# Kernel optimization log

Measured on AMD Instinct MI355X. Metric: run time of the kernel, lower is better.

The kernel has to match this reference:

```python
import jax, jax.numpy as jnp
import numpy as np

WS = 3          # windows_size
ND = 3          # num_dilation, dilations [1,2,3]
NSTATE = 16     # d_state
RANK = 12       # dt_rank = ceil(192/16)
TOPK = 36       # max(1,(20//3)**2)*depth
DM = 192        # d_model
DI = 384        # d_inner = 2*d_model
B0, HH, WW = 8, 96, 96


def setup_inputs() -> dict:
    ks = jax.random.split(jax.random.key(0), 12)
    f = jax.random.normal
    return {
        "x": f(ks[0], (B0, HH, WW, DM), jnp.float32),
        "W_in": f(ks[1], (2 * DI, DM), jnp.float32) * 0.02,
        "conv_w": f(ks[2], (DI, 1, 7, 7), jnp.float32) * 0.05,
        "conv_b": f(ks[3], (DI,), jnp.float32) * 0.01,
        "x_proj_w": f(ks[4], (2, RANK + 2 * NSTATE, DI), jnp.float32) * 0.02,
        "dt_w": f(ks[5], (2, DI, RANK), jnp.float32) * 0.02,
        "dt_b": f(ks[6], (2, DI), jnp.float32) * 0.01,
        "A_logs": jnp.tile(jnp.log(jnp.arange(1, NSTATE + 1, dtype=jnp.float32)), (2 * DI, 1)),
        "Ds": jnp.ones((2 * DI,), jnp.float32),
        "W_kv": f(ks[7], (2 * DI, DI), jnp.float32) * 0.02,
        "b_kv": jnp.zeros((2 * DI,), jnp.float32),
        "ln_g": jnp.ones((DI,), jnp.float32),
        "ln_b": jnp.zeros((DI,), jnp.float32),
        "W_out": f(ks[8], (DM, DI), jnp.float32) * 0.02,
    }


def _selective_scan(xs, x_proj_w, dt_w, dt_b, A_logs, Ds):
    # xs: (B, K=2, D, L) -> (B, K, D, L). Standard Mamba selective scan.
    B, K, D, L = xs.shape
    x_dbl = jnp.einsum('bkdl,kcd->bkcl', xs, x_proj_w)          # (B,K,R+2N,L)
    dts = x_dbl[:, :, :RANK]
    Bs = x_dbl[:, :, RANK:RANK + NSTATE]                        # (B,K,N,L)
    Cs = x_dbl[:, :, RANK + NSTATE:]                            # (B,K,N,L)
    delta = jax.nn.softplus(jnp.einsum('bkrl,kdr->bkdl', dts, dt_w) + dt_b[None, :, :, None])
    A = -jnp.exp(A_logs).reshape(K, D, NSTATE)
    dA = jnp.exp(delta[..., None] * A[None, :, :, None, :])    # (B,K,D,L,N)
    dBu = delta[..., None] * Bs.transpose(0, 1, 3, 2)[:, :, None, :, :] * xs[..., None]
    dA = jnp.moveaxis(dA, 3, 0)                                 # (L,B,K,D,N)
    dBu = jnp.moveaxis(dBu, 3, 0)
    C = jnp.moveaxis(Cs, 3, 0)                                  # (L,B,K,N)

    def step(h, inp):
        dA_t, dBu_t, C_t = inp
        h = dA_t * h + dBu_t
        y = jnp.einsum('bkdn,bkn->bkd', h, C_t)
        return h, y

    h0 = jnp.zeros((B, K, D, NSTATE), xs.dtype)
    _, ys = jax.lax.scan(step, h0, (dA, dBu, C))                # ys: (L,B,K,D)
    y = jnp.moveaxis(ys, 0, 3)                                  # (B,K,D,L)
    return y + Ds.reshape(1, K, D, 1) * xs


def _dynamic_mask_active(x):
    # x: (B,D,H,W). Partition into WSxWS windows, keep TOPK by mean activation.
    B, D, H, W = x.shape
    nH, nW = H // WS, W // WS
    w = x.reshape(B, D, nH, WS, nW, WS).transpose(0, 2, 4, 1, 3, 5)
    w = w.reshape(B, nH * nW, D, WS * WS)                       # (B,nWin,D,ws2)
    score = w.mean(axis=(2, 3))                                 # (B,nWin)
    _, idx = jax.lax.top_k(score, TOPK)                         # (B,TOPK)
    g = jnp.take_along_axis(w, idx[:, :, None, None], axis=1)   # (B,TOPK,D,ws2)
    return g.transpose(0, 2, 1, 3).reshape(B, D, TOPK * WS * WS)


def _unfold(x, d):
    # torch nn.Unfold(kernel=WS, dilation=d, padding=d, stride=1) on (B,C,H,W)
    B, C, H, W = x.shape
    xp = jnp.pad(x, ((0, 0), (0, 0), (d, d), (d, d)))
    pats = [xp[:, :, i * d:i * d + H, j * d:j * d + W] for i in range(WS) for j in range(WS)]
    p = jnp.stack(pats, axis=2)                                 # (B,C,ws2,H,W) channel-major like torch
    return p.reshape(B, C, WS * WS, H * W)


def _forward(x, W_in, conv_w, conv_b, x_proj_w, dt_w, dt_b, A_logs, Ds,
             W_kv, b_kv, ln_g, ln_b, W_out):
    B, H, W_, _ = x.shape
    xz = jnp.einsum('bhwc,oc->bhwo', x, W_in)
    xf, z = jnp.split(xz, 2, axis=-1)                           # (B,H,W,DI) each
    xc = xf.transpose(0, 3, 1, 2)
    xc = jax.lax.conv_general_dilated(xc, conv_w, (1, 1), [(3, 3), (3, 3)],
                                      feature_group_count=conv_w.shape[0],
                                      dimension_numbers=('NCHW', 'OIHW', 'NCHW'))
    xc = xc + conv_b[None, :, None, None]                       # (B,DI,H,W)
    D = xc.shape[1]

    # foreground SSM on active windows (forward + flipped scan)
    act = _dynamic_mask_active(xc)                              # (B,D,L)
    xs = jnp.stack([act, jnp.flip(act, axis=-1)], axis=1)       # (B,2,D,L)
    out = _selective_scan(xs, x_proj_w, dt_w, dt_b, A_logs, Ds)
    y1 = out[:, 0] + jnp.flip(out[:, 1], axis=-1)               # (B,D,L)
    y1 = y1.transpose(0, 2, 1)                                  # (B,L,D)

    L = y1.shape[1]
    ws2 = WS * WS
    n2 = L // ws2
    kv = jnp.einsum('bld,od->blo', y1, W_kv) + b_kv             # (B,L,2D)
    hd = 2 * D // ND
    t = kv.reshape(B, n2, ws2, ND, hd).transpose(3, 0, 4, 2, 1)  # (ND,B,hd,ws2,n2)
    Q, Kt = t[:, :, :hd // 2], t[:, :, hd // 2:]                 # (ND,B,D/ND,ws2,n2)

    dch = D // ND
    xr = xc.reshape(B, ND, dch, H, W_)
    ys = []
    for i in range(ND):
        V = _unfold(xr[:, i], i + 1)                            # (B,dch,ws2,n1)
        V = V.transpose(0, 1, 3, 2)                             # (B,dch,n1,ws2)
        s = jnp.einsum('bcwn,bcwn->bcw', Q[i], Kt[i]) / np.sqrt(dch).astype(np.float32)
        # softmax over a singleton axis (as in the source) -> all ones
        A_M = jax.nn.softmax(s[..., None], axis=-1)[..., 0]     # (B,dch,ws2)
        ys.append(jnp.einsum('bcnw,bcw->bcn', V, A_M))          # (B,dch,n1)
    y = jnp.concatenate(ys, axis=1)                             # (B,D,n1)
    y = y.transpose(0, 2, 1)                                    # (B,n1,D)

    mu = y.mean(-1, keepdims=True)
    var = y.var(-1, keepdims=True)
    y = (y - mu) / jnp.sqrt(var + 1e-5) * ln_g + ln_b
    y = y.reshape(B, H, W_, D) + z
    return jnp.einsum('bhwd,od->bhwo', y, W_out)


def reference(x, W_in, conv_w, conv_b, x_proj_w, dt_w, dt_b, A_logs, Ds,
              W_kv, b_kv, ln_g, ln_b, W_out):
    return _forward(x, W_in, conv_w, conv_b, x_proj_w, dt_w, dt_b, A_logs, Ds,
                    W_kv, b_kv, ln_g, ln_b, W_out)
```

## Files before the change

### kernel.cpp

```cpp
#include <hip/hip_runtime.h>
#include <cstddef>

#define B0V 8
#define HSV 96
#define WSV 96
#define DMV 192
#define DIV 384
#define MTOT (B0V*HSV*WSV)

typedef __attribute__((ext_vector_type(8))) unsigned short ushort8v;
typedef __attribute__((ext_vector_type(8))) short short8v;
typedef __attribute__((ext_vector_type(4))) float f32x4;
typedef _Float16 h2 __attribute__((ext_vector_type(2)));
typedef _Float16 h8 __attribute__((ext_vector_type(8)));

__device__ __forceinline__ unsigned short f2bf(float f) {
    unsigned int i; __builtin_memcpy(&i, &f, 4);
    i += 0x7FFFu + ((i >> 16) & 1);
    return (unsigned short)(i >> 16);
}

template<int ROWS>
__device__ __forceinline__ void stageBF16(const unsigned short* __restrict__ src, int ld,
                                          unsigned short* lds, int t) {
#pragma unroll
    for (int i = 0; i < ROWS*8/256; ++i) {
        const int cid = t + i*256;
        const int r = cid >> 3, cb = cid & 7;
        ushort8v sv = *(const ushort8v*)(src + (size_t)r*ld + cb*8);
        *(ushort8v*)((char*)lds + r*128 + ((cb ^ (r&7))<<4)) = sv;
    }
}
__device__ __forceinline__ short8v fragRead(const unsigned short* lds, int row, int kchunk) {
    return *(const short8v*)((const char*)lds + row*128 + ((kchunk ^ (row&7))<<4));
}

__global__ __launch_bounds__(256) void prep_kernel(
    const float* __restrict__ Wout, const float* __restrict__ Win,
    const float* __restrict__ cw,
    unsigned short* __restrict__ Wch, h2* __restrict__ w2h,
    unsigned short* __restrict__ WinfH, unsigned short* __restrict__ WoutH)
{
    const int blk = blockIdx.x;
    const int t = threadIdx.x;
    if (blk < 192) {
        __shared__ float wrow[384];
        for (int j = t; j < 384; j += 256) wrow[j] = Wout[(size_t)blk*384 + j];
        __syncthreads();
        if (t < 192) {
            float acc = 0.f;
#pragma unroll 4
            for (int j = 0; j < 384; ++j)
                acc += wrow[j] * Win[(size_t)(384 + j)*192 + t];
            Wch[(size_t)blk*192 + t] = f2bf(acc);
        }
    } else if (blk < 229) {
        const int idx = (blk - 192)*256 + t;
        if (idx < 49*192) {
            const int tap = idx / 192, cp = idx % 192;
            h2 v;
            v[0] = (_Float16)cw[(size_t)(2*cp  )*49 + tap];
            v[1] = (_Float16)cw[(size_t)(2*cp+1)*49 + tap];
            w2h[idx] = v;
        }
    } else if (blk < 265) {
        const int i = (blk - 229)*256 + t;
        if (i < 384*192/8) {
            const float4 f0 = *(const float4*)(Win + (size_t)i*8);
            const float4 f1 = *(const float4*)(Win + (size_t)i*8 + 4);
            ushort8v v;
            v[0]=f2bf(f0.x); v[1]=f2bf(f0.y); v[2]=f2bf(f0.z); v[3]=f2bf(f0.w);
            v[4]=f2bf(f1.x); v[5]=f2bf(f1.y); v[6]=f2bf(f1.z); v[7]=f2bf(f1.w);
            *(ushort8v*)(WinfH + (size_t)i*8) = v;
        }
    } else {
        const int i = (blk - 265)*256 + t;
        if (i < 192*384/8) {
            const float4 f0 = *(const float4*)(Wout + (size_t)i*8);
            const float4 f1 = *(const float4*)(Wout + (size_t)i*8 + 4);
            ushort8v v;
            v[0]=f2bf(f0.x); v[1]=f2bf(f0.y); v[2]=f2bf(f0.z); v[3]=f2bf(f0.w);
            v[4]=f2bf(f1.x); v[5]=f2bf(f1.y); v[6]=f2bf(f1.z); v[7]=f2bf(f1.w);
            *(ushort8v*)(WoutH + (size_t)i*8) = v;
        }
    }
}

__global__ __launch_bounds__(256) void gemm_in_mfma(
    const float* __restrict__ x, const unsigned short* __restrict__ Wh,
    unsigned short* __restrict__ xh, _Float16* __restrict__ xf)
{
    __shared__ unsigned short As[3*64*64];
    __shared__ unsigned short Bs[128*64];
    const int t = threadIdx.x;
    const int m0 = blockIdx.x * 64;
    const int wid = t >> 6, lane = t & 63;
    const int li = lane & 15, lg = lane >> 4;

#pragma unroll
    for (int kb = 0; kb < 3; ++kb) {
#pragma unroll
        for (int i = 0; i < 2; ++i) {
            const int cid = t + i*256;
            const int r = cid >> 3, cb = cid & 7;
            const float* p = x + (size_t)(m0 + r)*DMV + kb*64 + cb*8;
            float4 f0 = *(const float4*)p;
            float4 f1 = *(const float4*)(p+4);
            ushort8v sv;
            sv[0]=f2bf(f0.x); sv[1]=f2bf(f0.y); sv[2]=f2bf(f0.z); sv[3]=f2bf(f0.w);
            sv[4]=f2bf(f1.x); sv[5]=f2bf(f1.y); sv[6]=f2bf(f1.z); sv[7]=f2bf(f1.w);
            *(ushort8v*)((char*)(As + kb*64*64) + r*128 + ((cb ^ (r&7))<<4)) = sv;
            *(ushort8v*)(xh + (size_t)(m0 + r)*DMV + kb*64 + cb*8) = sv;
        }
    }

    for (int n0i = 0; n0i < 3; ++n0i) {
        const int n0 = n0i * 128;
        f32x4 acc[4][2];
#pragma unroll
        for (int i = 0; i < 4; ++i)
#pragma unroll
            for (int j = 0; j < 2; ++j) acc[i][j] = (f32x4){0.f,0.f,0.f,0.f};

        for (int kb = 0; kb < 3; ++kb) {
            __syncthreads();
            stageBF16<128>(Wh + (size_t)n0*DMV + kb*64, DMV, Bs, t);
            __syncthreads();
#pragma unroll
            for (int ks = 0; ks < 2; ++ks) {
                short8v a[4], b[2];
#pragma unroll
                for (int mf = 0; mf < 4; ++mf)
                    a[mf] = fragRead(As + kb*64*64, mf*16 + li, ks*4 + lg);
#pragma unroll
                for (int nf = 0; nf < 2; ++nf)
                    b[nf] = fragRead(Bs, wid*32 + nf*16 + li, ks*4 + lg);
#pragma unroll
                for (int mf = 0; mf < 4; ++mf)
#pragma unroll
                    for (int nf = 0; nf < 2; ++nf)
                        acc[mf][nf] = __builtin_amdgcn_mfma_f32_16x16x32_bf16(a[mf], b[nf], acc[mf][nf], 0, 0, 0);
            }
        }
#pragma unroll
        for (int mf = 0; mf < 4; ++mf)
#pragma unroll
            for (int nf = 0; nf < 2; ++nf)
#pragma unroll
                for (int i = 0; i < 4; ++i) {
                    const int row = m0 + mf*16 + lg*4 + i;
                    const int col = n0 + wid*32 + nf*16 + li;
                    xf[(size_t)row*DIV + col] = (_Float16)acc[mf][nf][i];
                }
    }
}

__global__ __launch_bounds__(256) void dwconv_kernel(
    const _Float16* __restrict__ xf, const h2* __restrict__ w2h,
    const float* __restrict__ cb, _Float16* __restrict__ xc)
{
    const int id  = blockIdx.x;
    const int swz = (id & 7) * 432 + (id >> 3);
    const int b    = swz / 432;
    const int rem  = swz - b*432;
    const int cg   = rem / 72;
    const int tile = rem - cg*72;
    const int th = tile / 6, tw = tile % 6;
    const int h0 = th*8, w0 = tw*16;
    const int c0 = cg*64;

    __shared__ _Float16 patch[14*22*64];
    const int t = threadIdx.x;
    for (int idx = t; idx < 308*8; idx += 256) {
        const int sp = idx >> 3, c8 = idx & 7;
        const int ih = sp / 22, iw = sp - ih*22;
        const int gh = h0 - 3 + ih, gw = w0 - 3 + iw;
        ushort8v v;
#pragma unroll
        for (int j = 0; j < 8; ++j) v[j] = 0;
        if ((unsigned)gh < (unsigned)HSV && (unsigned)gw < (unsigned)WSV)
            v = *(const ushort8v*)(xf + (((size_t)b*HSV + gh)*WSV + gw)*DIV + c0 + c8*8);
        *(ushort8v*)(patch + sp*64 + c8*8) = v;
    }
    __syncthreads();

    const int cp = t & 31;
    const int wq = t >> 5;

    h2 wreg[49];
    const h2* wp = w2h + (c0 >> 1) + cp;
#pragma unroll
    for (int k = 0; k < 49; ++k) wreg[k] = wp[k*192];

    h2 biasv;
    biasv[0] = (_Float16)cb[c0 + 2*cp];
    biasv[1] = (_Float16)cb[c0 + 2*cp + 1];
    h2 acc[8][2];
#pragma unroll
    for (int i = 0; i < 8; ++i) { acc[i][0] = biasv; acc[i][1] = biasv; }

    const h2* prow = (const h2*)patch;
#pragma unroll
    for (int ih = 0; ih < 14; ++ih) {
        h2 r[8];
#pragma unroll
        for (int j = 0; j < 8; ++j)
            r[j] = prow[(ih*22 + wq*2 + j)*32 + cp];
#pragma unroll
        for (int kw = 0; kw < 7; ++kw) {
#pragma unroll
            for (int oh = 0; oh < 8; ++oh) {
                const int kh = ih - oh;
                if (kh >= 0 && kh < 7) {
                    acc[oh][0] += wreg[kh*7 + kw] * r[kw];
                    acc[oh][1] += wreg[kh*7 + kw] * r[kw + 1];
                }
            }
        }
    }
    h2* xcp = (h2*)xc;
#pragma unroll
    for (int oh = 0; oh < 8; ++oh)
#pragma unroll
        for (int j = 0; j < 2; ++j)
            xcp[((((size_t)b*HSV + h0+oh)*WSV + (w0 + wq*2 + j))*DIV + c0)/2 + cp] = acc[oh][j];
}

__global__ __launch_bounds__(256) void boxln_kernel(
    const _Float16* __restrict__ xc,
    const float* __restrict__ g, const float* __restrict__ bta,
    unsigned short* __restrict__ yln)
{
    const int wid  = threadIdx.x >> 6;
    const int lane = threadIdx.x & 63;
    const int m = blockIdx.x * 4 + wid;
    const int b  = m / (HSV*WSV);
    const int hw = m % (HSV*WSV);
    const int h = hw / WSV, w = hw % WSV;

    const bool act = lane < 48;
    const int ch = lane * 8;
    const int dd = (ch >> 7) + 1;

    float s[8];
#pragma unroll
    for (int j = 0; j < 8; ++j) s[j] = 0.f;

#pragma unroll
    for (int a = -1; a <= 1; ++a)
#pragma unroll
        for (int bb = -1; bb <= 1; ++bb) {
            const int h2_ = h + a*dd, w2_ = w + bb*dd;
            if (act && (unsigned)h2_ < (unsigned)HSV && (unsigned)w2_ < (unsigned)WSV) {
                h8 v = *(const h8*)(xc + (((size_t)b*HSV + h2_)*WSV + w2_)*DIV + ch);
#pragma unroll
                for (int j = 0; j < 8; ++j) s[j] += (float)v[j];
            }
        }

    float ps = 0.f, ps2 = 0.f;
#pragma unroll
    for (int j = 0; j < 8; ++j) { ps += s[j]; ps2 += s[j]*s[j]; }
#pragma unroll
    for (int off = 32; off > 0; off >>= 1) {
        ps  += __shfl_xor(ps,  off);
        ps2 += __shfl_xor(ps2, off);
    }
    const float mu   = ps * (1.f/384.f);
    const float var  = ps2 * (1.f/384.f) - mu*mu;
    const float rstd = rsqrtf(var + 1e-5f);

    if (act) {
        float4 g0 = *(const float4*)(g + ch);
        float4 g1 = *(const float4*)(g + ch + 4);
        float4 b0 = *(const float4*)(bta + ch);
        float4 b1 = *(const float4*)(bta + ch + 4);
        float gv[8] = {g0.x,g0.y,g0.z,g0.w,g1.x,g1.y,g1.z,g1.w};
        float bv[8] = {b0.x,b0.y,b0.z,b0.w,b1.x,b1.y,b1.z,b1.w};
        ushort8v o;
#pragma unroll
        for (int j = 0; j < 8; ++j)
            o[j] = f2bf((s[j] - mu)*rstd*gv[j] + bv[j]);
        *(ushort8v*)(yln + (size_t)m*DIV + ch) = o;
    }
}

__global__ __launch_bounds__(256) void gemm_out_mfma(
    const unsigned short* __restrict__ Yl, const unsigned short* __restrict__ WoutH,
    const unsigned short* __restrict__ xh, const unsigned short* __restrict__ Wch,
    float* __restrict__ out)
{
    __shared__ unsigned short As[128*64];
    __shared__ unsigned short Bs[192*64];
    const int t = threadIdx.x;
    const int m0 = blockIdx.x * 128;
    const int wid = t >> 6, lane = t & 63;
    const int wm = wid >> 1, wn = wid & 1;
    const int li = lane & 15, lg = lane >> 4;

    f32x4 acc[4][6];
#pragma unroll
    for (int i = 0; i < 4; ++i)
#pragma unroll
        for (int j = 0; j < 6; ++j) acc[i][j] = (f32x4){0.f,0.f,0.f,0.f};

    for (int kb = 0; kb < 9; ++kb) {
        if (kb < 6) {
            stageBF16<128>(Yl + (size_t)m0*DIV + kb*64, DIV, As, t);
            stageBF16<192>(WoutH + kb*64, DIV, Bs, t);
        } else {
            stageBF16<128>(xh + (size_t)m0*DMV + (kb-6)*64, DMV, As, t);
            stageBF16<192>(Wch + (kb-6)*64, DMV, Bs, t);
        }
        __syncthreads();
#pragma unroll
        for (int ks = 0; ks < 2; ++ks) {
            short8v a[4], b[6];
#pragma unroll
            for (int mf = 0; mf < 4; ++mf) a[mf] = fragRead(As, wm*64 + mf*16 + li, ks*4 + lg);
#pragma unroll
            for (int nf = 0; nf < 6; ++nf) b[nf] = fragRead(Bs, wn*96 + nf*16 + li, ks*4 + lg);
#pragma unroll
            for (int mf = 0; mf < 4; ++mf)
#pragma unroll
                for (int nf = 0; nf < 6; ++nf)
                    acc[mf][nf] = __builtin_amdgcn_mfma_f32_16x16x32_bf16(a[mf], b[nf], acc[mf][nf], 0, 0, 0);
        }
        __syncthreads();
    }
#pragma unroll
    for (int mf = 0; mf < 4; ++mf)
#pragma unroll
        for (int nf = 0; nf < 6; ++nf)
#pragma unroll
            for (int i = 0; i < 4; ++i) {
                const int row = m0 + wm*64 + mf*16 + lg*4 + i;
                const int col = wn*96 + nf*16 + li;
                out[(size_t)row*DMV + col] = acc[mf][nf][i];
            }
}

extern "C" void kernel_launch(void* const* d_in, const int* in_sizes, int n_in,
                              void* d_out, int out_size, void* d_ws, size_t ws_size,
                              hipStream_t stream)
{
    const float* x      = (const float*)d_in[0];
    const float* W_in   = (const float*)d_in[1];
    const float* conv_w = (const float*)d_in[2];
    const float* conv_b = (const float*)d_in[3];
    const float* ln_g   = (const float*)d_in[11];
    const float* ln_b   = (const float*)d_in[12];
    const float* W_out  = (const float*)d_in[13];
    float* out = (float*)d_out;

    char* ws = (char*)d_ws;
    unsigned short* Wch   = (unsigned short*)(ws);
    h2*             w2h   = (h2*)(ws + 0x20000);
    unsigned short* WinfH = (unsigned short*)(ws + 0x40000);
    unsigned short* WoutH = (unsigned short*)(ws + 0x80000);
    unsigned short* xh    = (unsigned short*)(ws + 0x100000);
    _Float16*       xf    = (_Float16*)(ws + 0x2000000);
    _Float16*       xc    = (_Float16*)d_out;

    prep_kernel  <<<dim3(301),          256, 0, stream>>>(W_out, W_in, conv_w,
                                                          Wch, w2h, WinfH, WoutH);
    gemm_in_mfma <<<dim3(MTOT/64),      256, 0, stream>>>(x, WinfH, xh, xf);
    dwconv_kernel<<<dim3(3456),         256, 0, stream>>>(xf, w2h, conv_b, xc);
    boxln_kernel <<<dim3(MTOT/4),       256, 0, stream>>>(xc, ln_g, ln_b,
                                                          (unsigned short*)xf);
    gemm_out_mfma<<<dim3(MTOT/128),     256, 0, stream>>>((const unsigned short*)xf,
                                                          WoutH, xh, Wch, out);
}
```

Measured before the change: 191.3 us.

## Process two adjacent tiles per dwconv block with register-prefetched second patch

Each depthwise-conv block now handles two horizontally adjacent 8x16 output tiles instead of one, halving the grid. The second tile's input patch is loaded into registers while the first tile computes, then written to shared memory after a barrier. This aims to hide global-load latency and reuse the per-thread weight registers across two tiles. In exchange it adds 10 vector registers per thread, which may lower occupancy, and gives fewer blocks to spread across CUs.

```diff
diff --git a/kernel.cpp b/kernel.cpp
--- a/kernel.cpp
+++ b/kernel.cpp
@@ -160,21 +160,24 @@
     const float* __restrict__ cb, _Float16* __restrict__ xc)
 {
     const int id  = blockIdx.x;
-    const int swz = (id & 7) * 432 + (id >> 3);
-    const int b    = swz / 432;
-    const int rem  = swz - b*432;
+    const int swz = (id & 7) * 216 + (id >> 3);
+    const int T0  = swz * 2;
+    const int b    = T0 / 432;
+    const int rem  = T0 - b*432;
     const int cg   = rem / 72;
     const int tile = rem - cg*72;
     const int th = tile / 6, tw = tile % 6;
-    const int h0 = th*8, w0 = tw*16;
+    const int h0 = th*8;
+    const int w0a = tw*16, w0b = w0a + 16;
     const int c0 = cg*64;
 
     __shared__ _Float16 patch[14*22*64];
     const int t = threadIdx.x;
-    for (int idx = t; idx < 308*8; idx += 256) {
+
+    for (int idx = t; idx < 2464; idx += 256) {
         const int sp = idx >> 3, c8 = idx & 7;
         const int ih = sp / 22, iw = sp - ih*22;
-        const int gh = h0 - 3 + ih, gw = w0 - 3 + iw;
+        const int gh = h0 - 3 + ih, gw = w0a - 3 + iw;
         ushort8v v;
 #pragma unroll
         for (int j = 0; j < 8; ++j) v[j] = 0;
@@ -182,7 +185,23 @@
             v = *(const ushort8v*)(xf + (((size_t)b*HSV + gh)*WSV + gw)*DIV + c0 + c8*8);
         *(ushort8v*)(patch + sp*64 + c8*8) = v;
     }
-    __syncthreads();
+
+    ushort8v pre[10];
+#pragma unroll
+    for (int i = 0; i < 10; ++i) {
+        const int idx = t + i*256;
+        ushort8v v;
+#pragma unroll
+        for (int j = 0; j < 8; ++j) v[j] = 0;
+        if (idx < 2464) {
+            const int sp = idx >> 3, c8 = idx & 7;
+            const int ih = sp / 22, iw = sp - ih*22;
+            const int gh = h0 - 3 + ih, gw = w0b - 3 + iw;
+            if ((unsigned)gh < (unsigned)HSV && (unsigned)gw < (unsigned)WSV)
+                v = *(const ushort8v*)(xf + (((size_t)b*HSV + gh)*WSV + gw)*DIV + c0 + c8*8);
+        }
+        pre[i] = v;
+    }
 
     const int cp = t & 31;
     const int wq = t >> 5;
@@ -195,35 +214,53 @@
     h2 biasv;
     biasv[0] = (_Float16)cb[c0 + 2*cp];
     biasv[1] = (_Float16)cb[c0 + 2*cp + 1];
-    h2 acc[8][2];
-#pragma unroll
-    for (int i = 0; i < 8; ++i) { acc[i][0] = biasv; acc[i][1] = biasv; }
-
+
+    h2* xcp = (h2*)xc;
     const h2* prow = (const h2*)patch;
-#pragma unroll
-    for (int ih = 0; ih < 14; ++ih) {
-        h2 r[8];
-#pragma unroll
-        for (int j = 0; j < 8; ++j)
-            r[j] = prow[(ih*22 + wq*2 + j)*32 + cp];
-#pragma unroll
-        for (int kw = 0; kw < 7; ++kw) {
-#pragma unroll
-            for (int oh = 0; oh < 8; ++oh) {
-                const int kh = ih - oh;
-                if (kh >= 0 && kh < 7) {
-                    acc[oh][0] += wreg[kh*7 + kw] * r[kw];
-                    acc[oh][1] += wreg[kh*7 + kw] * r[kw + 1];
+
+    auto compute_store = [&](int w0) {
+        h2 acc[8][2];
+#pragma unroll
+        for (int i = 0; i < 8; ++i) { acc[i][0] = biasv; acc[i][1] = biasv; }
+#pragma unroll
+        for (int ih = 0; ih < 14; ++ih) {
+            h2 r[8];
+#pragma unroll
+            for (int j = 0; j < 8; ++j)
+                r[j] = prow[(ih*22 + wq*2 + j)*32 + cp];
+#pragma unroll
+            for (int kw = 0; kw < 7; ++kw) {
+#pragma unroll
+                for (int oh = 0; oh < 8; ++oh) {
+                    const int kh = ih - oh;
+                    if (kh >= 0 && kh < 7) {
+                        acc[oh][0] += wreg[kh*7 + kw] * r[kw];
+                        acc[oh][1] += wreg[kh*7 + kw] * r[kw + 1];
+                    }
                 }
             }
         }
-    }
-    h2* xcp = (h2*)xc;
-#pragma unroll
-    for (int oh = 0; oh < 8; ++oh)
-#pragma unroll
-        for (int j = 0; j < 2; ++j)
-            xcp[((((size_t)b*HSV + h0+oh)*WSV + (w0 + wq*2 + j))*DIV + c0)/2 + cp] = acc[oh][j];
+#pragma unroll
+        for (int oh = 0; oh < 8; ++oh)
+#pragma unroll
+            for (int j = 0; j < 2; ++j)
+                xcp[((((size_t)b*HSV + h0+oh)*WSV + (w0 + wq*2 + j))*DIV + c0)/2 + cp] = acc[oh][j];
+    };
+
+    __syncthreads();
+    compute_store(w0a);
+    __syncthreads();
+
+#pragma unroll
+    for (int i = 0; i < 10; ++i) {
+        const int idx = t + i*256;
+        if (idx < 2464) {
+            const int sp = idx >> 3, c8 = idx & 7;
+            *(ushort8v*)(patch + sp*64 + c8*8) = pre[i];
+        }
+    }
+    __syncthreads();
+    compute_store(w0b);
 }
 
 __global__ __launch_bounds__(256) void boxln_kernel(
@@ -365,7 +402,7 @@
     prep_kernel  <<<dim3(301),          256, 0, stream>>>(W_out, W_in, conv_w,
                                                           Wch, w2h, WinfH, WoutH);
     gemm_in_mfma <<<dim3(MTOT/64),      256, 0, stream>>>(x, WinfH, xh, xf);
-    dwconv_kernel<<<dim3(3456),         256, 0, stream>>>(xf, w2h, conv_b, xc);
+    dwconv_kernel<<<dim3(1728),         256, 0, stream>>>(xf, w2h, conv_b, xc);
     boxln_kernel <<<dim3(MTOT/4),       256, 0, stream>>>(xc, ln_g, ln_b,
                                                           (unsigned short*)xf);
     gemm_out_mfma<<<dim3(MTOT/128),     256, 0, stream>>>((const unsigned short*)xf,
```

New measurement: 197.3 us. 1.03x slower.
